# Kernel optimization log

Hardware: AMD Instinct MI355X
Metric: run time of the kernel (lower is better)

Reference implementation:

```python
import jax, jax.numpy as jnp
import numpy as np

HIDDEN = 2048
N_HEADS = 16
N_KV = 4
HEAD_DIM = 128
B, T = 2, 2048


def setup_inputs() -> dict:
    key = jax.random.key(0)
    k1, k2, k3, k4 = jax.random.split(key, 4)
    x = jax.random.normal(k1, (B, T, HIDDEN), dtype=jnp.float32)
    # linear weights stored [out, in] like torch; we apply x @ W.T
    w_q = jax.random.normal(k2, (N_HEADS * HEAD_DIM, HIDDEN), dtype=jnp.float32) * (HIDDEN ** -0.5)
    w_kv = jax.random.normal(k3, (2 * N_KV * HEAD_DIM, HIDDEN), dtype=jnp.float32) * (HIDDEN ** -0.5)
    w_o = jax.random.normal(k4, (HIDDEN, N_HEADS * HEAD_DIM), dtype=jnp.float32) * ((N_HEADS * HEAD_DIM) ** -0.5)
    return {"x": x, "w_q": w_q, "w_kv": w_kv, "w_o": w_o}


def reference(x, w_q, w_kv, w_o):
    b, t, _ = x.shape
    groups = N_HEADS // N_KV
    scale = HEAD_DIM ** -0.5

    q = (x @ w_q.T).reshape(b, t, N_HEADS, HEAD_DIM).transpose(0, 2, 1, 3)  # [B,H,T,D]
    kv = x @ w_kv.T
    k, v = jnp.split(kv, 2, axis=-1)
    k = k.reshape(b, t, N_KV, HEAD_DIM).transpose(0, 2, 1, 3)  # [B,KV,T,D]
    v = v.reshape(b, t, N_KV, HEAD_DIM).transpose(0, 2, 1, 3)
    # repeat_interleave over head dim -> [B,H,T,D]
    k = jnp.repeat(k, groups, axis=1)
    v = jnp.repeat(v, groups, axis=1)

    scores = jnp.einsum('bhqd,bhkd->bhqk', q, k) * scale  # [B,H,T,T]
    causal = jnp.triu(jnp.ones((t, t), dtype=bool), k=1)
    scores = jnp.where(causal, -jnp.inf, scores)
    weights = jax.nn.softmax(scores, axis=-1)
    out = jnp.einsum('bhqk,bhkd->bhqd', weights, v)  # [B,H,T,D]
    out = out.transpose(0, 2, 1, 3).reshape(b, t, N_HEADS * HEAD_DIM)
    return out @ w_o.T
```

## Files before the change

### kernel.cpp

```cpp
#include <hip/hip_runtime.h>

typedef short bf16x8 __attribute__((ext_vector_type(8)));
typedef float f32x4 __attribute__((ext_vector_type(4)));

__device__ __forceinline__ unsigned short f2bf(float f) {
    unsigned int u = __float_as_uint(f);
    u = (u + 0x7fff + ((u >> 16) & 1)) >> 16;
    return (unsigned short)u;
}
__device__ __forceinline__ float bf2f(short s) {
    return __uint_as_float(((unsigned int)(unsigned short)s) << 16);
}

__device__ __forceinline__ void async16(const void* g, void* l) {
    __builtin_amdgcn_global_load_lds(
        (const __attribute__((address_space(1))) void*)g,
        (__attribute__((address_space(3))) void*)l,
        16 , 0 , 0 );
}

__global__ void castk(const float* __restrict__ in, unsigned short* __restrict__ out, int n4) {
    int i = blockIdx.x * blockDim.x + threadIdx.x;
    if (i < n4) {
        float4 f = ((const float4*)in)[i];
        ushort4 u;
        u.x = f2bf(f.x); u.y = f2bf(f.y); u.z = f2bf(f.z); u.w = f2bf(f.w);
        ((ushort4*)out)[i] = u;
    }
}

template <typename OutT>
__global__ __launch_bounds__(256) void gemm_bt(const unsigned short* __restrict__ A,
                                               const unsigned short* __restrict__ B,
                                               OutT* __restrict__ C,
                                               int M, int N, int K,
                                               int ncut, float qscale) {
    __shared__ unsigned short As[128 * 32];
    __shared__ unsigned short Bs[128 * 32];
    const int tid  = threadIdx.x;
    const int lane = tid & 63;
    const int w    = tid >> 6;
    const int quad = lane >> 4;
    const int l16  = lane & 15;
    const int wr   = w >> 1;
    const int wc   = w & 1;
    const int m0 = blockIdx.x * 128;
    const int n0 = blockIdx.y * 128;

    f32x4 acc[4][4] = {};

    const int srow = 16 * w + (lane >> 2);
    const int scol = (lane & 3) * 8;
    const unsigned short* Ag = A + (size_t)(m0 + srow) * K + scol;
    const unsigned short* Bg = B + (size_t)(n0 + srow) * K + scol;
    unsigned short* AsW = &As[(16 * w) * 32];
    unsigned short* BsW = &Bs[(16 * w) * 32];

    for (int k0 = 0; k0 < K; k0 += 32) {
        async16(Ag + k0,                  AsW);
        async16(Ag + (size_t)64 * K + k0, AsW + 64 * 32);
        async16(Bg + k0,                  BsW);
        async16(Bg + (size_t)64 * K + k0, BsW + 64 * 32);
        __syncthreads();

        bf16x8 af[4], bfr[4];
#pragma unroll
        for (int mt = 0; mt < 4; ++mt)
            af[mt] = *(const bf16x8*)&As[(wr * 64 + mt * 16 + l16) * 32 + quad * 8];
#pragma unroll
        for (int nt = 0; nt < 4; ++nt)
            bfr[nt] = *(const bf16x8*)&Bs[(wc * 64 + nt * 16 + l16) * 32 + quad * 8];
#pragma unroll
        for (int mt = 0; mt < 4; ++mt)
#pragma unroll
            for (int nt = 0; nt < 4; ++nt)
                acc[mt][nt] = __builtin_amdgcn_mfma_f32_16x16x32_bf16(af[mt], bfr[nt], acc[mt][nt], 0, 0, 0);
        __syncthreads();
    }

#pragma unroll
    for (int mt = 0; mt < 4; ++mt) {
        int row = m0 + wr * 64 + mt * 16 + quad * 4;
#pragma unroll
        for (int nt = 0; nt < 4; ++nt) {
            int col = n0 + wc * 64 + nt * 16 + l16;
            f32x4 v = acc[mt][nt];
            float s = (col < ncut) ? qscale : 1.0f;
#pragma unroll
            for (int j = 0; j < 4; ++j) {
                float vj = v[j] * s;
                if constexpr (sizeof(OutT) == 4)
                    C[(size_t)(row + j) * N + col] = vj;
                else
                    C[(size_t)(row + j) * N + col] = f2bf(vj);
            }
        }
    }
}

__global__ __launch_bounds__(256) void transpose_v(const unsigned short* __restrict__ QKV,
                                                   unsigned short* __restrict__ Vt) {
    __shared__ unsigned short Ls[64 * 136];
    const int tid = threadIdx.x;
    const int k0  = blockIdx.x * 64;
    const int b   = blockIdx.y >> 2;
    const int kvh = blockIdx.y & 3;

#pragma unroll
    for (int pass = 0; pass < 4; ++pass) {
        int c = tid + pass * 256;
        int key = c >> 4, dc = (c & 15) * 8;
        bf16x8 v = *(const bf16x8*)(QKV + (size_t)(b * 2048 + k0 + key) * 3072 + 2560 + kvh * 128 + dc);
        *(bf16x8*)&Ls[key * 136 + dc] = v;
    }
    __syncthreads();
#pragma unroll
    for (int pass = 0; pass < 4; ++pass) {
        int c = tid + pass * 256;
        int d = c >> 3, kc = (c & 7) * 8;
        bf16x8 v;
#pragma unroll
        for (int i = 0; i < 8; ++i) v[i] = (short)Ls[(kc + i) * 136 + d];
        *(bf16x8*)(Vt + ((size_t)(b * 4 + kvh) * 128 + d) * 2048 + k0 + kc) = v;
    }
}

__global__ __launch_bounds__(256, 4) void attn_fwd4(const unsigned short* __restrict__ QKV,
                                                    const unsigned short* __restrict__ Vt,
                                                    unsigned short* __restrict__ Opart,
                                                    float* __restrict__ lpart) {
    __shared__ unsigned short Ks[64 * 136];
    __shared__ unsigned short Vs[128 * 72];

    const int tid  = threadIdx.x;
    const int lane = tid & 63;
    const int w    = tid >> 6;
    const int quad = lane >> 4;
    const int l16  = lane & 15;

    const int hb   = blockIdx.x;
    const int h    = hb & 15;
    const int b    = hb >> 4;
    const int y    = blockIdx.y;
    const int p    = 31 - (y >> 1);
    const int half = y & 1;
    const int kvh  = h >> 2;
    const float M_FIX = 12.0f;

    const int ntot   = p + 1;
    const int mid    = (p + 2) >> 1;
    const int tstart = half ? mid : 0;
    const int tend   = half ? ntot : mid;

    const int qw = p * 64 + w * 16;

    bf16x8 qf[4];
#pragma unroll
    for (int kd = 0; kd < 4; ++kd)
        qf[kd] = *(const bf16x8*)(QKV + (size_t)(b * 2048 + qw + l16) * 3072 + h * 128 + kd * 32 + quad * 8);

    f32x4 oacc[8] = {};
    float rs[4] = {0.f, 0.f, 0.f, 0.f};

    unsigned short* Pw = &Ks[w * 1152];
    const size_t vtbase = ((size_t)(b * 4 + kvh) * 128) * 2048;

    for (int t = tstart; t < tend; ++t) {
        const int k0 = t * 64;
#pragma unroll
        for (int pass = 0; pass < 4; ++pass) {
            int c = tid + pass * 256;
            int key = c >> 4, dc = (c & 15) * 8;
            bf16x8 kv = *(const bf16x8*)(QKV + (size_t)(b * 2048 + k0 + key) * 3072 + 2048 + kvh * 128 + dc);
            *(bf16x8*)&Ks[key * 136 + dc] = kv;
            int d = c >> 3, kc = (c & 7) * 8;
            bf16x8 vv = *(const bf16x8*)(Vt + vtbase + (size_t)d * 2048 + k0 + kc);
            *(bf16x8*)&Vs[d * 72 + kc] = vv;
        }
        __syncthreads();

        f32x4 sacc[4] = {};
#pragma unroll
        for (int kt = 0; kt < 4; ++kt)
#pragma unroll
            for (int kd = 0; kd < 4; ++kd) {
                bf16x8 kf = *(const bf16x8*)&Ks[(kt * 16 + l16) * 136 + kd * 32 + quad * 8];
                sacc[kt] = __builtin_amdgcn_mfma_f32_16x16x32_bf16(qf[kd], kf, sacc[kt], 0, 0, 0);
            }
        __syncthreads();

        const bool diag = (t == p);
#pragma unroll
        for (int j = 0; j < 4; ++j) {
            int qrow = qw + quad * 4 + j;
#pragma unroll
            for (int kt = 0; kt < 4; ++kt) {
                float pv = __expf(sacc[kt][j] - M_FIX);
                if (diag) {
                    int key = k0 + kt * 16 + l16;
                    if (key > qrow) pv = 0.f;
                }
                rs[j] += pv;
                Pw[(quad * 4 + j) * 72 + kt * 16 + l16] = f2bf(pv);
            }
        }

#pragma unroll
        for (int ks = 0; ks < 2; ++ks) {
            bf16x8 pf = *(const bf16x8*)&Pw[l16 * 72 + ks * 32 + quad * 8];
#pragma unroll
            for (int dt = 0; dt < 8; ++dt) {
                bf16x8 vf = *(const bf16x8*)&Vs[(dt * 16 + l16) * 72 + ks * 32 + quad * 8];
                oacc[dt] = __builtin_amdgcn_mfma_f32_16x16x32_bf16(pf, vf, oacc[dt], 0, 0, 0);
            }
        }
        __syncthreads();
    }

#pragma unroll
    for (int j = 0; j < 4; ++j) {
        float r = rs[j];
#pragma unroll
        for (int off = 1; off < 16; off <<= 1)
            r += __shfl_xor(r, off, 64);
        if (l16 == 0)
            lpart[((size_t)(half * 2 + b) * 16 + h) * 2048 + qw + quad * 4 + j] = r;
    }
#pragma unroll
    for (int dt = 0; dt < 8; ++dt)
#pragma unroll
        for (int j = 0; j < 4; ++j) {
            int qrow = qw + quad * 4 + j;
            Opart[(size_t)(half * 4096 + b * 2048 + qrow) * 2048 + h * 128 + dt * 16 + l16] =
                f2bf(oacc[dt][j]);
        }
}

__global__ __launch_bounds__(256) void combine(const unsigned short* __restrict__ Opart,
                                               const float* __restrict__ lpart,
                                               unsigned short* __restrict__ O) {
    const int r   = blockIdx.x;
    const int b   = r >> 11, row = r & 2047;
    const int col = threadIdx.x * 8;
    const int h   = col >> 7;
    bf16x8 a = *(const bf16x8*)(Opart + (size_t)r * 2048 + col);
    bf16x8 c = *(const bf16x8*)(Opart + (size_t)(4096 + r) * 2048 + col);
    float la = lpart[((size_t)(0 * 2 + b) * 16 + h) * 2048 + row];
    float lb = lpart[((size_t)(1 * 2 + b) * 16 + h) * 2048 + row];
    float inv = 1.0f / (la + lb);
    bf16x8 o;
#pragma unroll
    for (int i = 0; i < 8; ++i)
        o[i] = (short)f2bf((bf2f(a[i]) + bf2f(c[i])) * inv);
    *(bf16x8*)(O + (size_t)r * 2048 + col) = o;
}

extern "C" void kernel_launch(void* const* d_in, const int* in_sizes, int n_in,
                              void* d_out, int out_size, void* d_ws, size_t ws_size,
                              hipStream_t stream) {
    const float* x   = (const float*)d_in[0];
    const float* wq  = (const float*)d_in[1];
    const float* wkv = (const float*)d_in[2];
    const float* wo  = (const float*)d_in[3];
    float* out = (float*)d_out;

    char* ws = (char*)d_ws;
    size_t off = 0;
    auto alloc = [&](size_t bytes) { size_t o = off; off += (bytes + 255) & ~(size_t)255; return o; };
    unsigned short* xb    = (unsigned short*)(ws + alloc((size_t)4096 * 2048 * 2));
    unsigned short* wqkvb = (unsigned short*)(ws + alloc((size_t)3072 * 2048 * 2));
    unsigned short* wob   = (unsigned short*)(ws + alloc((size_t)2048 * 2048 * 2));
    unsigned short* QKVb  = (unsigned short*)(ws + alloc((size_t)4096 * 3072 * 2));
    unsigned short* Ab    = (unsigned short*)(ws + alloc((size_t)4096 * 2048 * 2));
    unsigned short* Vtb   = (unsigned short*)(ws + alloc((size_t)2 * 4 * 128 * 2048 * 2));
    unsigned short* Opart = (unsigned short*)(ws + alloc((size_t)2 * 4096 * 2048 * 2));
    float*          lpart = (float*)(ws + alloc((size_t)2 * 2 * 16 * 2048 * 4));

    const float qscale = 0.08838834764831845f;

    castk<<<8192, 256, 0, stream>>>(x,   xb,    4096 * 2048 / 4);
    castk<<<4096, 256, 0, stream>>>(wq,  wqkvb, 2048 * 2048 / 4);
    castk<<<2048, 256, 0, stream>>>(wkv, wqkvb + (size_t)2048 * 2048, 1024 * 2048 / 4);
    castk<<<4096, 256, 0, stream>>>(wo,  wob,   2048 * 2048 / 4);

    gemm_bt<unsigned short><<<dim3(32, 24), 256, 0, stream>>>(xb, wqkvb, QKVb, 4096, 3072, 2048, 2048, qscale);

    transpose_v<<<dim3(32, 8), 256, 0, stream>>>(QKVb, Vtb);

    attn_fwd4<<<dim3(32, 64), 256, 0, stream>>>(QKVb, Vtb, Opart, lpart);
    combine<<<4096, 256, 0, stream>>>(Opart, lpart, Ab);

    gemm_bt<float><<<dim3(32, 16), 256, 0, stream>>>(Ab, wob, out, 4096, 2048, 2048, 0, 1.0f);
}
```

Measured before the change: 337.0 us.

## Double-buffer async K/V loads with 128-row query tiles and swizzled LDS

Replaces the attention kernel with a version that streams K and V tiles into two LDS buffers using direct global-to-LDS async loads, so the next tile loads while the current one is computed. Each block now covers 128 query rows, with each warp handling two 16-row groups that share the K/V fragments, and causally dead tiles are skipped per warp. Padded LDS layouts are replaced by XOR swizzles, and MFMA sections are wrapped in raised wave priority. The larger LDS footprint and register use cut occupancy to 2 blocks per CU, and the split-K halves now divide work in 64-key tiles over a 128-row query block.

```diff
diff --git a/kernel.cpp b/kernel.cpp
--- a/kernel.cpp
+++ b/kernel.cpp
@@ -125,115 +125,178 @@
     }
 }
 
-__global__ __launch_bounds__(256, 4) void attn_fwd4(const unsigned short* __restrict__ QKV,
+__global__ __launch_bounds__(256, 2) void attn_fwd5(const unsigned short* __restrict__ QKV,
                                                     const unsigned short* __restrict__ Vt,
                                                     unsigned short* __restrict__ Opart,
                                                     float* __restrict__ lpart) {
-    __shared__ unsigned short Ks[64 * 136];
-    __shared__ unsigned short Vs[128 * 72];
+    __shared__ __attribute__((aligned(16))) unsigned short Ks[2][64 * 128];
+    __shared__ __attribute__((aligned(16))) unsigned short Vs[2][128 * 64];
+    __shared__ __attribute__((aligned(16))) unsigned short Ps[4][32 * 64];
 
     const int tid  = threadIdx.x;
     const int lane = tid & 63;
     const int w    = tid >> 6;
     const int quad = lane >> 4;
     const int l16  = lane & 15;
+    const int swz  = (l16 & 7) << 3;
 
     const int hb   = blockIdx.x;
     const int h    = hb & 15;
     const int b    = hb >> 4;
     const int y    = blockIdx.y;
-    const int p    = 31 - (y >> 1);
+    const int p    = 15 - (y >> 1);
     const int half = y & 1;
     const int kvh  = h >> 2;
     const float M_FIX = 12.0f;
 
     const int ntot   = p + 1;
-    const int mid    = (p + 2) >> 1;
-    const int tstart = half ? mid : 0;
-    const int tend   = half ? ntot : mid;
-
-    const int qw = p * 64 + w * 16;
-
-    bf16x8 qf[4];
-#pragma unroll
-    for (int kd = 0; kd < 4; ++kd)
-        qf[kd] = *(const bf16x8*)(QKV + (size_t)(b * 2048 + qw + l16) * 3072 + h * 128 + kd * 32 + quad * 8);
-
-    f32x4 oacc[8] = {};
-    float rs[4] = {0.f, 0.f, 0.f, 0.f};
-
-    unsigned short* Pw = &Ks[w * 1152];
-    const size_t vtbase = ((size_t)(b * 4 + kvh) * 128) * 2048;
+    const int tstart = half ? ntot : 0;
+    const int tend   = half ? 2 * ntot : ntot;
+
+    const int qbase = p * 128;
+    const int qw0   = qbase + w * 32;
+    const int qw1   = qw0 + 16;
+
+    bf16x8 qf[2][4];
+#pragma unroll
+    for (int g = 0; g < 2; ++g)
+#pragma unroll
+        for (int kd = 0; kd < 4; ++kd)
+            qf[g][kd] = *(const bf16x8*)(QKV + (size_t)(b * 2048 + qw0 + g * 16 + l16) * 3072
+                                         + h * 128 + kd * 32 + quad * 8);
+
+    f32x4 oacc[2][8] = {};
+    float rs[2][4] = {};
+
+    const unsigned short* gk[4];
+    const unsigned short* gv[4];
+#pragma unroll
+    for (int pp = 0; pp < 4; ++pp) {
+        int r  = (4 * w + pp) * 4 + (lane >> 4);
+        int s  = lane & 15;
+        int sp = (s & 8) | ((s ^ r) & 7);
+        gk[pp] = QKV + (size_t)(b * 2048 + r) * 3072 + 2048 + kvh * 128 + sp * 8;
+        int d  = (4 * w + pp) * 8 + (lane >> 3);
+        int sv = (lane & 7) ^ (d & 7);
+        gv[pp] = Vt + ((size_t)(b * 4 + kvh) * 128 + d) * 2048 + sv * 8;
+    }
+
+    unsigned short* Pw = &Ps[w][0];
+
+    auto stage = [&](int nb, int t) {
+        const size_t ko = (size_t)t * 64;
+#pragma unroll
+        for (int pp = 0; pp < 4; ++pp) {
+            async16(gk[pp] + ko * 3072, &Ks[nb][(4 * w + pp) * 512]);
+            async16(gv[pp] + ko,        &Vs[nb][(4 * w + pp) * 512]);
+        }
+    };
+
+    stage(0, tstart);
+    int cur = 0;
 
     for (int t = tstart; t < tend; ++t) {
+        __syncthreads();
+        if (t + 1 < tend) stage(cur ^ 1, t + 1);
         const int k0 = t * 64;
-#pragma unroll
-        for (int pass = 0; pass < 4; ++pass) {
-            int c = tid + pass * 256;
-            int key = c >> 4, dc = (c & 15) * 8;
-            bf16x8 kv = *(const bf16x8*)(QKV + (size_t)(b * 2048 + k0 + key) * 3072 + 2048 + kvh * 128 + dc);
-            *(bf16x8*)&Ks[key * 136 + dc] = kv;
-            int d = c >> 3, kc = (c & 7) * 8;
-            bf16x8 vv = *(const bf16x8*)(Vt + vtbase + (size_t)d * 2048 + k0 + kc);
-            *(bf16x8*)&Vs[d * 72 + kc] = vv;
+
+        if (k0 <= qw0 + 15) {
+            const bool live1 = (k0 <= qw1 + 15);
+
+            f32x4 sacc[2][4] = {};
+            __builtin_amdgcn_s_setprio(1);
+#pragma unroll
+            for (int kt = 0; kt < 4; ++kt) {
+                bf16x8 kf[4];
+#pragma unroll
+                for (int kd = 0; kd < 4; ++kd)
+                    kf[kd] = *(const bf16x8*)&Ks[cur][(kt * 16 + l16) * 128
+                                                      + ((kd * 32 + quad * 8) ^ swz)];
+#pragma unroll
+                for (int kd = 0; kd < 4; ++kd)
+                    sacc[0][kt] = __builtin_amdgcn_mfma_f32_16x16x32_bf16(qf[0][kd], kf[kd], sacc[0][kt], 0, 0, 0);
+                if (live1) {
+#pragma unroll
+                    for (int kd = 0; kd < 4; ++kd)
+                        sacc[1][kt] = __builtin_amdgcn_mfma_f32_16x16x32_bf16(qf[1][kd], kf[kd], sacc[1][kt], 0, 0, 0);
+                }
+            }
+            __builtin_amdgcn_s_setprio(0);
+
+#pragma unroll
+            for (int g = 0; g < 2; ++g) {
+                if (g == 1 && !live1) continue;
+                const int qwg = qw0 + g * 16;
+                const bool diag = (k0 + 63 > qwg);
+#pragma unroll
+                for (int j = 0; j < 4; ++j) {
+                    int qrow = qwg + quad * 4 + j;
+                    int prow = g * 16 + quad * 4 + j;
+                    int psw  = (prow & 7) << 3;
+#pragma unroll
+                    for (int kt = 0; kt < 4; ++kt) {
+                        float pv = __expf(sacc[g][kt][j] - M_FIX);
+                        if (diag) {
+                            int key = k0 + kt * 16 + l16;
+                            if (key > qrow) pv = 0.f;
+                        }
+                        rs[g][j] += pv;
+                        Pw[prow * 64 + ((kt * 16 + l16) ^ psw)] = f2bf(pv);
+                    }
+                }
+            }
+
+            bf16x8 pf[2][2];
+#pragma unroll
+            for (int g = 0; g < 2; ++g) {
+                if (g == 1 && !live1) continue;
+#pragma unroll
+                for (int ks = 0; ks < 2; ++ks)
+                    pf[g][ks] = *(const bf16x8*)&Pw[(g * 16 + l16) * 64
+                                                    + ((ks * 32 + quad * 8) ^ swz)];
+            }
+            __builtin_amdgcn_s_setprio(1);
+#pragma unroll
+            for (int dt = 0; dt < 8; ++dt) {
+                bf16x8 vf[2];
+#pragma unroll
+                for (int ks = 0; ks < 2; ++ks)
+                    vf[ks] = *(const bf16x8*)&Vs[cur][(dt * 16 + l16) * 64
+                                                      + ((ks * 32 + quad * 8) ^ swz)];
+#pragma unroll
+                for (int ks = 0; ks < 2; ++ks)
+                    oacc[0][dt] = __builtin_amdgcn_mfma_f32_16x16x32_bf16(pf[0][ks], vf[ks], oacc[0][dt], 0, 0, 0);
+                if (live1) {
+#pragma unroll
+                    for (int ks = 0; ks < 2; ++ks)
+                        oacc[1][dt] = __builtin_amdgcn_mfma_f32_16x16x32_bf16(pf[1][ks], vf[ks], oacc[1][dt], 0, 0, 0);
+                }
+            }
+            __builtin_amdgcn_s_setprio(0);
         }
-        __syncthreads();
-
-        f32x4 sacc[4] = {};
-#pragma unroll
-        for (int kt = 0; kt < 4; ++kt)
-#pragma unroll
-            for (int kd = 0; kd < 4; ++kd) {
-                bf16x8 kf = *(const bf16x8*)&Ks[(kt * 16 + l16) * 136 + kd * 32 + quad * 8];
-                sacc[kt] = __builtin_amdgcn_mfma_f32_16x16x32_bf16(qf[kd], kf, sacc[kt], 0, 0, 0);
-            }
-        __syncthreads();
-
-        const bool diag = (t == p);
+        cur ^= 1;
+    }
+
+#pragma unroll
+    for (int g = 0; g < 2; ++g) {
 #pragma unroll
         for (int j = 0; j < 4; ++j) {
-            int qrow = qw + quad * 4 + j;
-#pragma unroll
-            for (int kt = 0; kt < 4; ++kt) {
-                float pv = __expf(sacc[kt][j] - M_FIX);
-                if (diag) {
-                    int key = k0 + kt * 16 + l16;
-                    if (key > qrow) pv = 0.f;
-                }
-                rs[j] += pv;
-                Pw[(quad * 4 + j) * 72 + kt * 16 + l16] = f2bf(pv);
-            }
+            float r = rs[g][j];
+#pragma unroll
+            for (int off = 1; off < 16; off <<= 1)
+                r += __shfl_xor(r, off, 64);
+            if (l16 == 0)
+                lpart[((size_t)(half * 2 + b) * 16 + h) * 2048 + qw0 + g * 16 + quad * 4 + j] = r;
         }
-
-#pragma unroll
-        for (int ks = 0; ks < 2; ++ks) {
-            bf16x8 pf = *(const bf16x8*)&Pw[l16 * 72 + ks * 32 + quad * 8];
-#pragma unroll
-            for (int dt = 0; dt < 8; ++dt) {
-                bf16x8 vf = *(const bf16x8*)&Vs[(dt * 16 + l16) * 72 + ks * 32 + quad * 8];
-                oacc[dt] = __builtin_amdgcn_mfma_f32_16x16x32_bf16(pf, vf, oacc[dt], 0, 0, 0);
-            }
-        }
-        __syncthreads();
-    }
-
-#pragma unroll
-    for (int j = 0; j < 4; ++j) {
-        float r = rs[j];
-#pragma unroll
-        for (int off = 1; off < 16; off <<= 1)
-            r += __shfl_xor(r, off, 64);
-        if (l16 == 0)
-            lpart[((size_t)(half * 2 + b) * 16 + h) * 2048 + qw + quad * 4 + j] = r;
-    }
-#pragma unroll
-    for (int dt = 0; dt < 8; ++dt)
-#pragma unroll
-        for (int j = 0; j < 4; ++j) {
-            int qrow = qw + quad * 4 + j;
-            Opart[(size_t)(half * 4096 + b * 2048 + qrow) * 2048 + h * 128 + dt * 16 + l16] =
-                f2bf(oacc[dt][j]);
-        }
+#pragma unroll
+        for (int dt = 0; dt < 8; ++dt)
+#pragma unroll
+            for (int j = 0; j < 4; ++j) {
+                int qrow = qw0 + g * 16 + quad * 4 + j;
+                Opart[(size_t)(half * 4096 + b * 2048 + qrow) * 2048 + h * 128 + dt * 16 + l16] =
+                    f2bf(oacc[g][dt][j]);
+            }
+    }
 }
 
 __global__ __launch_bounds__(256) void combine(const unsigned short* __restrict__ Opart,
@@ -287,7 +350,7 @@
 
     transpose_v<<<dim3(32, 8), 256, 0, stream>>>(QKVb, Vtb);
 
-    attn_fwd4<<<dim3(32, 64), 256, 0, stream>>>(QKVb, Vtb, Opart, lpart);
+    attn_fwd5<<<dim3(32, 32), 256, 0, stream>>>(QKVb, Vtb, Opart, lpart);
     combine<<<4096, 256, 0, stream>>>(Opart, lpart, Ab);
 
     gemm_bt<float><<<dim3(32, 16), 256, 0, stream>>>(Ab, wob, out, 4096, 2048, 2048, 0, 1.0f);
```

Result: faster. 311.3 us (-7.6%).
